# Performance work log

Measured on AMD Instinct MI355X. Metric: run time of the kernel, lower is better.

The kernel has to match this reference:

```python
import jax, jax.numpy as jnp
import numpy as np

EXP, MAN = 8, 23  # exponent/mantissa bits of the simulated float format


def float_quantize(x, exp=EXP, man=MAN):
    """Round-to-nearest-even quantization to a float format with `exp` exponent
    bits and `man` mantissa bits (faithful to mptorch float_quantize 'nearest').
    With exp=8, man=23 this is an exact identity on fp32 inputs."""
    emax = 2 ** (exp - 1) - 1          # max unbiased exponent
    emin = 1 - emax                     # min normal exponent (clamping here yields subnormal grid)
    ax = jnp.abs(x)
    e = jnp.clip(jnp.floor(jnp.log2(jnp.where(ax > 0, ax, 1.0))), emin, emax)
    # scale mantissa into [1,2), round to `man` fractional bits (ties-to-even via jnp.round)
    m = jnp.round(x * jnp.exp2(-e) * (2.0 ** man)) * (2.0 ** -man)
    q = m * jnp.exp2(e)
    maxval = (2.0 - 2.0 ** -man) * (2.0 ** emax)
    q = jnp.clip(q, -maxval, maxval)
    return jnp.where(ax == 0, x, q).astype(x.dtype)


def setup_inputs() -> dict:
    key = jax.random.key(0)
    k1, k2, k3 = jax.random.split(key, 3)
    M, IN, OUT = 8192, 1024, 4096
    x = jax.random.normal(k1, (M, IN), dtype=jnp.float32)
    # kaiming-uniform-ish scale for weight, 1/sqrt(fan_in) for bias
    bound_w = float(np.sqrt(1.0 / IN))
    weight = jax.random.uniform(k2, (OUT, IN), dtype=jnp.float32, minval=-bound_w, maxval=bound_w)
    bias = jax.random.uniform(k3, (OUT,), dtype=jnp.float32, minval=-bound_w, maxval=bound_w)
    return {"x": x, "weight": weight, "bias": bias}


def reference(x, weight, bias):
    # QLinearFunction.forward: quantize weight, quant_gemm, add quantized bias, quantize output.
    # quant_gemm with (man=23, exp=8) simulates fp32 multiply-accumulate, i.e. a plain
    # fp32 GEMM; we express it as matmul followed by output quantization.
    qweight = float_quantize(weight)                 # [OUT, IN]
    out = jnp.matmul(x, qweight.T)                   # [M, OUT], fp32 accumulate
    out = out + float_quantize(bias)[None, :]
    return float_quantize(out)
```

## Files before the change

kernel.cpp:

```cpp
#include <hip/hip_runtime.h>
#include <stdint.h>

#define MM 8192
#define KK 1024
#define NN 4096
#define NT 32
#define TE 8192
#define PL 16384

typedef float f32x4 __attribute__((ext_vector_type(4)));
typedef __bf16 bf16x8 __attribute__((ext_vector_type(8)));
typedef unsigned short u16x8 __attribute__((ext_vector_type(8)));

static __device__ __forceinline__ unsigned short f2bf(float f) {
    unsigned int u = __builtin_bit_cast(unsigned int, f);
    u += 0x7fffu + ((u >> 16) & 1u);
    return (unsigned short)(u >> 16);
}
static __device__ __forceinline__ float bf2f(unsigned short s) {
    unsigned int u = ((unsigned int)s) << 16;
    return __builtin_bit_cast(float, u);
}

__global__ __launch_bounds__(256) void split_pack(const float* __restrict__ in,
        unsigned short* __restrict__ hi, unsigned short* __restrict__ lo, int total) {
    int i = blockIdx.x * 256 + threadIdx.x;
    if (i >= total) return;
    int row = i >> 7;
    int og  = i & 127;
    int kt  = og >> 2, oct = og & 3;
    int bt  = row >> 8, r = row & 255;
    const float4* s = (const float4*)(in + (size_t)row * KK + kt * 32 + oct * 8);
    float4 a = s[0], b = s[1];
    float v[8] = {a.x, a.y, a.z, a.w, b.x, b.y, b.z, b.w};
    u16x8 h, l;
#pragma unroll
    for (int j = 0; j < 8; ++j) {
        unsigned short hb = f2bf(v[j]);
        h[j] = hb;
        l[j] = f2bf(v[j] - bf2f(hb));
    }
    int slot = r * 4 + (oct ^ ((r >> 1) & 3));
    size_t off = (size_t)(bt * NT + kt) * TE + (size_t)slot * 8;
    *(u16x8*)(hi + off) = h;
    *(u16x8*)(lo + off) = l;
}

static __device__ __forceinline__ bf16x8 ldsr(unsigned addr) {
    bf16x8 r;
    asm volatile("ds_read_b128 %0, %1" : "=v"(r) : "v"(addr));
    return r;
}
static __device__ __forceinline__ void gl16(const unsigned short* g, unsigned short* l) {
    __builtin_amdgcn_global_load_lds(
        (__attribute__((address_space(1))) void*)(void*)g,
        (__attribute__((address_space(3))) void*)(void*)l, 16, 0, 0);
}
static __device__ __forceinline__ void mf(f32x4& d, bf16x8 a, bf16x8 b) {
    d = __builtin_amdgcn_mfma_f32_16x16x32_bf16(a, b, d, 0, 0, 0);
}

#define PHASE_PRE() \
    __builtin_amdgcn_s_barrier(); \
    asm volatile("s_waitcnt lgkmcnt(0)" ::: "memory"); \
    __builtin_amdgcn_sched_barrier(0); \
    __builtin_amdgcn_s_setprio(1);
#define PHASE_POST() \
    __builtin_amdgcn_s_setprio(0); \
    __builtin_amdgcn_s_barrier();
#define CLUSTER(M0, M1) \
    _Pragma("unroll") \
    for (int ni = 0; ni < 4; ++ni) { \
        mf(acc[M0][ni], a0, bh[ni]); mf(acc[M0][ni], l0, bh[ni]); mf(acc[M0][ni], a0, blo[ni]); \
        mf(acc[M1][ni], a1, bh[ni]); mf(acc[M1][ni], l1, bh[ni]); mf(acc[M1][ni], a1, blo[ni]); \
    }

__global__ __launch_bounds__(512, 2) void qlinear_mfma(
        const unsigned short* __restrict__ Ah, const unsigned short* __restrict__ Al,
        const unsigned short* __restrict__ Bh, const unsigned short* __restrict__ Bl,
        const float* __restrict__ bias, float* __restrict__ out) {
    __shared__ __attribute__((aligned(16))) unsigned short S[2][4][TE];

    int bid = blockIdx.x;
    int wg = (bid & 7) * 64 + (bid >> 3);
    int bm = wg & 31, bn = wg >> 5;

    const int tix = threadIdx.x;
    const int lane = tix & 63, wid = tix >> 6;
    const int wr = (wid >> 2) * 128, wc = (wid & 3) * 64;
    const int lr = lane & 15, lg = lane >> 4;
    const int xorv = (lr >> 1) & 3;

    const unsigned lb = (unsigned)(uintptr_t)(__attribute__((address_space(3))) void*)&S[0][0][0];
    const unsigned pA = lb + (unsigned)(((wr + lr) * 32 + (lg ^ xorv) * 8) * 2);
    const unsigned pB = lb + (unsigned)(((wc + lr) * 32 + (lg ^ xorv) * 8) * 2);

    const int soff = wid * 1024 + lane * 8;
    const unsigned short* sAh = Ah + (size_t)bm * NT * TE + soff;
    const unsigned short* sAl = Al + (size_t)bm * NT * TE + soff;
    const unsigned short* sBh = Bh + (size_t)bn * NT * TE + soff;
    const unsigned short* sBl = Bl + (size_t)bn * NT * TE + soff;

    f32x4 acc[8][4];
#pragma unroll
    for (int mi = 0; mi < 8; ++mi)
#pragma unroll
        for (int ni = 0; ni < 4; ++ni) acc[mi][ni] = (f32x4){0.f, 0.f, 0.f, 0.f};

    gl16(sAh,       &S[0][0][wid * 1024]);
    gl16(sAh + 512, &S[0][0][wid * 1024 + 512]);
    gl16(sAl,       &S[0][1][wid * 1024]);
    gl16(sAl + 512, &S[0][1][wid * 1024 + 512]);
    gl16(sBh,       &S[0][2][wid * 1024]);
    gl16(sBh + 512, &S[0][2][wid * 1024 + 512]);
    gl16(sBl,       &S[0][3][wid * 1024]);
    gl16(sBl + 512, &S[0][3][wid * 1024 + 512]);
    asm volatile("s_waitcnt vmcnt(0)" ::: "memory");
    __builtin_amdgcn_s_barrier();

    for (int t = 0; t < NT; ++t) {
        const unsigned bo = (unsigned)(t & 1) * (4 * PL);
        const int nb = (t & 1) ^ 1;
        const size_t st = (size_t)(t + 1) * TE;
        const bool pf = (t + 1 < NT);

        bf16x8 bh[4], blo[4], a0, a1, l0, l1;

#pragma unroll
        for (int ni = 0; ni < 4; ++ni) {
            bh[ni]  = ldsr(pB + bo + 2 * PL + ni * 1024);
            blo[ni] = ldsr(pB + bo + 3 * PL + ni * 1024);
        }
        a0 = ldsr(pA + bo);        l0 = ldsr(pA + bo + PL);
        a1 = ldsr(pA + bo + 1024); l1 = ldsr(pA + bo + PL + 1024);
        if (pf) {
            gl16(sAh + st,       &S[nb][0][wid * 1024]);
            gl16(sAh + st + 512, &S[nb][0][wid * 1024 + 512]);
            gl16(sAl + st,       &S[nb][1][wid * 1024]);
            gl16(sAl + st + 512, &S[nb][1][wid * 1024 + 512]);
        }
        PHASE_PRE();
        CLUSTER(0, 1);
        PHASE_POST();

        a0 = ldsr(pA + bo + 2 * 1024); l0 = ldsr(pA + bo + PL + 2 * 1024);
        a1 = ldsr(pA + bo + 3 * 1024); l1 = ldsr(pA + bo + PL + 3 * 1024);
        if (pf) {
            gl16(sBh + st,       &S[nb][2][wid * 1024]);
            gl16(sBh + st + 512, &S[nb][2][wid * 1024 + 512]);
            gl16(sBl + st,       &S[nb][3][wid * 1024]);
            gl16(sBl + st + 512, &S[nb][3][wid * 1024 + 512]);
        }
        PHASE_PRE();
        CLUSTER(2, 3);
        PHASE_POST();

        a0 = ldsr(pA + bo + 4 * 1024); l0 = ldsr(pA + bo + PL + 4 * 1024);
        a1 = ldsr(pA + bo + 5 * 1024); l1 = ldsr(pA + bo + PL + 5 * 1024);
        PHASE_PRE();
        CLUSTER(4, 5);
        PHASE_POST();

        a0 = ldsr(pA + bo + 6 * 1024); l0 = ldsr(pA + bo + PL + 6 * 1024);
        a1 = ldsr(pA + bo + 7 * 1024); l1 = ldsr(pA + bo + PL + 7 * 1024);
        PHASE_PRE();
        CLUSTER(6, 7);
        __builtin_amdgcn_s_setprio(0);
        asm volatile("s_waitcnt vmcnt(0)" ::: "memory");
        __builtin_amdgcn_s_barrier();
    }

    const int row0 = bm * 256 + wr + lg * 4;
    const int col0 = bn * 256 + wc + lr;
    float bv[4];
#pragma unroll
    for (int ni = 0; ni < 4; ++ni) bv[ni] = bias[col0 + ni * 16];
#pragma unroll
    for (int mi = 0; mi < 8; ++mi)
#pragma unroll
        for (int ni = 0; ni < 4; ++ni) {
            float* o = out + (size_t)(row0 + mi * 16) * NN + col0 + ni * 16;
#pragma unroll
            for (int r = 0; r < 4; ++r)
                o[(size_t)r * NN] = acc[mi][ni][r] + bv[ni];
        }
}

__global__ __launch_bounds__(256) void qlinear_naive(const float* __restrict__ x,
                                                     const float* __restrict__ w,
                                                     const float* __restrict__ bias,
                                                     float* __restrict__ out) {
    int n = blockIdx.x * 64 + (threadIdx.x & 63);
    int m = blockIdx.y * 4 + (threadIdx.x >> 6);
    const float4* xr = (const float4*)(x + (size_t)m * KK);
    const float4* wr = (const float4*)(w + (size_t)n * KK);
    float s = 0.f;
    for (int k = 0; k < KK / 4; ++k) {
        float4 a = xr[k], b = wr[k];
        s += a.x * b.x + a.y * b.y + a.z * b.z + a.w * b.w;
    }
    out[(size_t)m * NN + n] = s + bias[n];
}

extern "C" void kernel_launch(void* const* d_in, const int* in_sizes, int n_in,
                              void* d_out, int out_size, void* d_ws, size_t ws_size,
                              hipStream_t stream) {
    (void)in_sizes; (void)n_in; (void)out_size;
    const float* x = (const float*)d_in[0];
    const float* w = (const float*)d_in[1];
    const float* bias = (const float*)d_in[2];
    float* out = (float*)d_out;

    const size_t xcnt = (size_t)MM * KK;
    const size_t wcnt = (size_t)NN * KK;
    const size_t need = (xcnt + wcnt) * 2 * sizeof(unsigned short);

    if (ws_size >= need) {
        unsigned short* xh = (unsigned short*)d_ws;
        unsigned short* xl = xh + xcnt;
        unsigned short* wh = xl + xcnt;
        unsigned short* wl = wh + wcnt;
        split_pack<<<(int)(MM * 128 / 256), 256, 0, stream>>>(x, xh, xl, MM * 128);
        split_pack<<<(int)(NN * 128 / 256), 256, 0, stream>>>(w, wh, wl, NN * 128);
        qlinear_mfma<<<512, 512, 0, stream>>>(xh, xl, wh, wl, bias, out);
    } else {
        dim3 grid(NN / 64, MM / 4);
        qlinear_naive<<<grid, 256, 0, stream>>>(x, w, bias, out);
    }
}
```

Baseline: 335.3 us.

## Switch GEMM to 256x128 tiles with triple-buffered LDS pipeline

Output tiles go from 256x256 to 256x128, so the grid doubles to 1024 blocks and each wave keeps 8x2 accumulators. A three-stage LDS ring issues global loads two K-steps ahead, synchronised with vmcnt waits, replacing double buffering and the per-phase barriers. The split/pack kernel now writes output contiguously and gathers its inputs with swizzled source addresses, so B is packed per 128-row tile. The intent is to hide load latency and cut barrier overhead. In exchange, B reuse per block drops, more of A must be streamed, and occupancy falls to one block per CU.

```diff
diff --git a/kernel.cpp b/kernel.cpp
--- a/kernel.cpp
+++ b/kernel.cpp
@@ -5,8 +5,9 @@
 #define KK 1024
 #define NN 4096
 #define NT 32
-#define TE 8192
-#define PL 16384
+#define TEA 8192
+#define TEB 4096
+#define BUFE 24576
 
 typedef float f32x4 __attribute__((ext_vector_type(4)));
 typedef __bf16 bf16x8 __attribute__((ext_vector_type(8)));
@@ -23,27 +24,28 @@
 }
 
 __global__ __launch_bounds__(256) void split_pack(const float* __restrict__ in,
-        unsigned short* __restrict__ hi, unsigned short* __restrict__ lo, int total) {
-    int i = blockIdx.x * 256 + threadIdx.x;
-    if (i >= total) return;
-    int row = i >> 7;
-    int og  = i & 127;
-    int kt  = og >> 2, oct = og & 3;
-    int bt  = row >> 8, r = row & 255;
-    const float4* s = (const float4*)(in + (size_t)row * KK + kt * 32 + oct * 8);
-    float4 a = s[0], b = s[1];
+        unsigned short* __restrict__ hi, unsigned short* __restrict__ lo,
+        int R, int spl, int total) {
+    int j = blockIdx.x * 256 + threadIdx.x;
+    if (j >= total) return;
+    int p = j >> spl;
+    int s = j & ((R * 4) - 1);
+    int r = s >> 2;
+    int oct = (s & 3) ^ ((r >> 1) & 3);
+    int bt = p >> 5, kt = p & 31;
+    size_t src = (size_t)(bt * R + r) * KK + kt * 32 + oct * 8;
+    const float4* sp = (const float4*)(in + src);
+    float4 a = sp[0], b = sp[1];
     float v[8] = {a.x, a.y, a.z, a.w, b.x, b.y, b.z, b.w};
     u16x8 h, l;
 #pragma unroll
-    for (int j = 0; j < 8; ++j) {
-        unsigned short hb = f2bf(v[j]);
-        h[j] = hb;
-        l[j] = f2bf(v[j] - bf2f(hb));
-    }
-    int slot = r * 4 + (oct ^ ((r >> 1) & 3));
-    size_t off = (size_t)(bt * NT + kt) * TE + (size_t)slot * 8;
-    *(u16x8*)(hi + off) = h;
-    *(u16x8*)(lo + off) = l;
+    for (int q = 0; q < 8; ++q) {
+        unsigned short hb = f2bf(v[q]);
+        h[q] = hb;
+        l[q] = f2bf(v[q] - bf2f(hb));
+    }
+    *(u16x8*)(hi + (size_t)j * 8) = h;
+    *(u16x8*)(lo + (size_t)j * 8) = l;
 }
 
 static __device__ __forceinline__ bf16x8 ldsr(unsigned addr) {
@@ -60,125 +62,113 @@
     d = __builtin_amdgcn_mfma_f32_16x16x32_bf16(a, b, d, 0, 0, 0);
 }
 
-#define PHASE_PRE() \
-    __builtin_amdgcn_s_barrier(); \
-    asm volatile("s_waitcnt lgkmcnt(0)" ::: "memory"); \
-    __builtin_amdgcn_sched_barrier(0); \
-    __builtin_amdgcn_s_setprio(1);
-#define PHASE_POST() \
-    __builtin_amdgcn_s_setprio(0); \
-    __builtin_amdgcn_s_barrier();
-#define CLUSTER(M0, M1) \
-    _Pragma("unroll") \
-    for (int ni = 0; ni < 4; ++ni) { \
-        mf(acc[M0][ni], a0, bh[ni]); mf(acc[M0][ni], l0, bh[ni]); mf(acc[M0][ni], a0, blo[ni]); \
-        mf(acc[M1][ni], a1, bh[ni]); mf(acc[M1][ni], l1, bh[ni]); mf(acc[M1][ni], a1, blo[ni]); \
-    }
-
-__global__ __launch_bounds__(512, 2) void qlinear_mfma(
+__global__ __launch_bounds__(512, 1) void qlinear_mfma(
         const unsigned short* __restrict__ Ah, const unsigned short* __restrict__ Al,
         const unsigned short* __restrict__ Bh, const unsigned short* __restrict__ Bl,
         const float* __restrict__ bias, float* __restrict__ out) {
-    __shared__ __attribute__((aligned(16))) unsigned short S[2][4][TE];
+    __shared__ __attribute__((aligned(16))) unsigned short S[3 * BUFE];
 
     int bid = blockIdx.x;
-    int wg = (bid & 7) * 64 + (bid >> 3);
-    int bm = wg & 31, bn = wg >> 5;
+    int wg = (bid & 7) * 128 + (bid >> 3);
+    int bm = wg >> 5, bn = wg & 31;
 
     const int tix = threadIdx.x;
     const int lane = tix & 63, wid = tix >> 6;
-    const int wr = (wid >> 2) * 128, wc = (wid & 3) * 64;
+    const int wr = (wid >> 2) * 128;
+    const int wc = (wid & 3) * 32;
     const int lr = lane & 15, lg = lane >> 4;
     const int xorv = (lr >> 1) & 3;
 
-    const unsigned lb = (unsigned)(uintptr_t)(__attribute__((address_space(3))) void*)&S[0][0][0];
-    const unsigned pA = lb + (unsigned)(((wr + lr) * 32 + (lg ^ xorv) * 8) * 2);
-    const unsigned pB = lb + (unsigned)(((wc + lr) * 32 + (lg ^ xorv) * 8) * 2);
-
-    const int soff = wid * 1024 + lane * 8;
-    const unsigned short* sAh = Ah + (size_t)bm * NT * TE + soff;
-    const unsigned short* sAl = Al + (size_t)bm * NT * TE + soff;
-    const unsigned short* sBh = Bh + (size_t)bn * NT * TE + soff;
-    const unsigned short* sBl = Bl + (size_t)bn * NT * TE + soff;
-
-    f32x4 acc[8][4];
+    const unsigned lb = (unsigned)(uintptr_t)(__attribute__((address_space(3))) void*)&S[0];
+    const unsigned pA = (unsigned)(((wr + lr) * 32 + (lg ^ xorv) * 8) * 2);
+    const unsigned pB = (unsigned)(((wc + lr) * 32 + (lg ^ xorv) * 8) * 2);
+
+    const unsigned short* pAh = Ah + (size_t)bm * NT * TEA + wid * 1024 + lane * 8;
+    const unsigned short* pAl = Al + (size_t)bm * NT * TEA + wid * 1024 + lane * 8;
+    const unsigned short* pBh = Bh + (size_t)bn * NT * TEB + wid * 512 + lane * 8;
+    const unsigned short* pBl = Bl + (size_t)bn * NT * TEB + wid * 512 + lane * 8;
+
+#define STAGE(T, SOF) do {                                                   \
+        unsigned short* db = &S[(SOF)];                                      \
+        size_t ta = (size_t)(T) * TEA, tb = (size_t)(T) * TEB;               \
+        gl16(pAh + ta,       db + wid * 1024);                               \
+        gl16(pAh + ta + 512, db + wid * 1024 + 512);                         \
+        gl16(pAl + ta,       db + 8192 + wid * 1024);                        \
+        gl16(pAl + ta + 512, db + 8192 + wid * 1024 + 512);                  \
+        gl16(pBh + tb,       db + 16384 + wid * 512);                        \
+        gl16(pBl + tb,       db + 20480 + wid * 512);                        \
+    } while (0)
+
+    f32x4 acc[8][2];
+#pragma unroll
+    for (int mi = 0; mi < 8; ++mi) {
+        acc[mi][0] = (f32x4){0.f, 0.f, 0.f, 0.f};
+        acc[mi][1] = (f32x4){0.f, 0.f, 0.f, 0.f};
+    }
+
+    STAGE(0, 0);
+    STAGE(1, BUFE);
+
+    unsigned roff = 0;
+    unsigned soff = 2 * BUFE;
+
+    for (int t = 0; t < NT; ++t) {
+        if (t == NT - 1) asm volatile("s_waitcnt vmcnt(0)" ::: "memory");
+        else             asm volatile("s_waitcnt vmcnt(6)" ::: "memory");
+        __builtin_amdgcn_s_barrier();
+
+        if (t < NT - 2) STAGE(t + 2, soff);
+
+        const unsigned ab = lb + roff * 2 + pA;
+        const unsigned bb = lb + roff * 2 + 32768 + pB;
+
+        bf16x8 ah[8], al[8], bh2[2], bl2[2];
+        bh2[0] = ldsr(bb);          bh2[1] = ldsr(bb + 1024);
+        bl2[0] = ldsr(bb + 8192);   bl2[1] = ldsr(bb + 8192 + 1024);
+#pragma unroll
+        for (int mi = 0; mi < 4; ++mi) {
+            ah[mi] = ldsr(ab + mi * 1024);
+            al[mi] = ldsr(ab + 16384 + mi * 1024);
+        }
+#pragma unroll
+        for (int mi = 4; mi < 8; ++mi) {
+            ah[mi] = ldsr(ab + mi * 1024);
+            al[mi] = ldsr(ab + 16384 + mi * 1024);
+        }
+
+        asm volatile("s_waitcnt lgkmcnt(8)" ::: "memory");
+        __builtin_amdgcn_sched_barrier(0);
+        __builtin_amdgcn_s_setprio(1);
+#pragma unroll
+        for (int mi = 0; mi < 4; ++mi) { mf(acc[mi][0], ah[mi], bh2[0]); mf(acc[mi][1], ah[mi], bh2[1]); }
+#pragma unroll
+        for (int mi = 0; mi < 4; ++mi) { mf(acc[mi][0], al[mi], bh2[0]); mf(acc[mi][1], al[mi], bh2[1]); }
+#pragma unroll
+        for (int mi = 0; mi < 4; ++mi) { mf(acc[mi][0], ah[mi], bl2[0]); mf(acc[mi][1], ah[mi], bl2[1]); }
+
+        asm volatile("s_waitcnt lgkmcnt(0)" ::: "memory");
+        __builtin_amdgcn_sched_barrier(0);
+#pragma unroll
+        for (int mi = 4; mi < 8; ++mi) { mf(acc[mi][0], ah[mi], bh2[0]); mf(acc[mi][1], ah[mi], bh2[1]); }
+#pragma unroll
+        for (int mi = 4; mi < 8; ++mi) { mf(acc[mi][0], al[mi], bh2[0]); mf(acc[mi][1], al[mi], bh2[1]); }
+#pragma unroll
+        for (int mi = 4; mi < 8; ++mi) { mf(acc[mi][0], ah[mi], bl2[0]); mf(acc[mi][1], ah[mi], bl2[1]); }
+        __builtin_amdgcn_s_setprio(0);
+        __builtin_amdgcn_sched_barrier(0);
+
+        roff = (roff == 2 * BUFE) ? 0u : roff + BUFE;
+        soff = (soff == 2 * BUFE) ? 0u : soff + BUFE;
+    }
+#undef STAGE
+
+    const int row0 = bm * 256 + wr + lg * 4;
+    const int col0 = bn * 128 + wc + lr;
+    float bv[2] = {bias[col0], bias[col0 + 16]};
 #pragma unroll
     for (int mi = 0; mi < 8; ++mi)
 #pragma unroll
-        for (int ni = 0; ni < 4; ++ni) acc[mi][ni] = (f32x4){0.f, 0.f, 0.f, 0.f};
-
-    gl16(sAh,       &S[0][0][wid * 1024]);
-    gl16(sAh + 512, &S[0][0][wid * 1024 + 512]);
-    gl16(sAl,       &S[0][1][wid * 1024]);
-    gl16(sAl + 512, &S[0][1][wid * 1024 + 512]);
-    gl16(sBh,       &S[0][2][wid * 1024]);
-    gl16(sBh + 512, &S[0][2][wid * 1024 + 512]);
-    gl16(sBl,       &S[0][3][wid * 1024]);
-    gl16(sBl + 512, &S[0][3][wid * 1024 + 512]);
-    asm volatile("s_waitcnt vmcnt(0)" ::: "memory");
-    __builtin_amdgcn_s_barrier();
-
-    for (int t = 0; t < NT; ++t) {
-        const unsigned bo = (unsigned)(t & 1) * (4 * PL);
-        const int nb = (t & 1) ^ 1;
-        const size_t st = (size_t)(t + 1) * TE;
-        const bool pf = (t + 1 < NT);
-
-        bf16x8 bh[4], blo[4], a0, a1, l0, l1;
-
-#pragma unroll
-        for (int ni = 0; ni < 4; ++ni) {
-            bh[ni]  = ldsr(pB + bo + 2 * PL + ni * 1024);
-            blo[ni] = ldsr(pB + bo + 3 * PL + ni * 1024);
-        }
-        a0 = ldsr(pA + bo);        l0 = ldsr(pA + bo + PL);
-        a1 = ldsr(pA + bo + 1024); l1 = ldsr(pA + bo + PL + 1024);
-        if (pf) {
-            gl16(sAh + st,       &S[nb][0][wid * 1024]);
-            gl16(sAh + st + 512, &S[nb][0][wid * 1024 + 512]);
-            gl16(sAl + st,       &S[nb][1][wid * 1024]);
-            gl16(sAl + st + 512, &S[nb][1][wid * 1024 + 512]);
-        }
-        PHASE_PRE();
-        CLUSTER(0, 1);
-        PHASE_POST();
-
-        a0 = ldsr(pA + bo + 2 * 1024); l0 = ldsr(pA + bo + PL + 2 * 1024);
-        a1 = ldsr(pA + bo + 3 * 1024); l1 = ldsr(pA + bo + PL + 3 * 1024);
-        if (pf) {
-            gl16(sBh + st,       &S[nb][2][wid * 1024]);
-            gl16(sBh + st + 512, &S[nb][2][wid * 1024 + 512]);
-            gl16(sBl + st,       &S[nb][3][wid * 1024]);
-            gl16(sBl + st + 512, &S[nb][3][wid * 1024 + 512]);
-        }
-        PHASE_PRE();
-        CLUSTER(2, 3);
-        PHASE_POST();
-
-        a0 = ldsr(pA + bo + 4 * 1024); l0 = ldsr(pA + bo + PL + 4 * 1024);
-        a1 = ldsr(pA + bo + 5 * 1024); l1 = ldsr(pA + bo + PL + 5 * 1024);
-        PHASE_PRE();
-        CLUSTER(4, 5);
-        PHASE_POST();
-
-        a0 = ldsr(pA + bo + 6 * 1024); l0 = ldsr(pA + bo + PL + 6 * 1024);
-        a1 = ldsr(pA + bo + 7 * 1024); l1 = ldsr(pA + bo + PL + 7 * 1024);
-        PHASE_PRE();
-        CLUSTER(6, 7);
-        __builtin_amdgcn_s_setprio(0);
-        asm volatile("s_waitcnt vmcnt(0)" ::: "memory");
-        __builtin_amdgcn_s_barrier();
-    }
-
-    const int row0 = bm * 256 + wr + lg * 4;
-    const int col0 = bn * 256 + wc + lr;
-    float bv[4];
-#pragma unroll
-    for (int ni = 0; ni < 4; ++ni) bv[ni] = bias[col0 + ni * 16];
-#pragma unroll
-    for (int mi = 0; mi < 8; ++mi)
-#pragma unroll
-        for (int ni = 0; ni < 4; ++ni) {
+        for (int ni = 0; ni < 2; ++ni) {
             float* o = out + (size_t)(row0 + mi * 16) * NN + col0 + ni * 16;
 #pragma unroll
             for (int r = 0; r < 4; ++r)
@@ -220,9 +210,9 @@
         unsigned short* xl = xh + xcnt;
         unsigned short* wh = xl + xcnt;
         unsigned short* wl = wh + wcnt;
-        split_pack<<<(int)(MM * 128 / 256), 256, 0, stream>>>(x, xh, xl, MM * 128);
-        split_pack<<<(int)(NN * 128 / 256), 256, 0, stream>>>(w, wh, wl, NN * 128);
-        qlinear_mfma<<<512, 512, 0, stream>>>(xh, xl, wh, wl, bias, out);
+        split_pack<<<(int)(xcnt / 8 / 256), 256, 0, stream>>>(x, xh, xl, 256, 10, (int)(xcnt / 8));
+        split_pack<<<(int)(wcnt / 8 / 256), 256, 0, stream>>>(w, wh, wl, 128, 9, (int)(wcnt / 8));
+        qlinear_mfma<<<1024, 512, 0, stream>>>(xh, xl, wh, wl, bias, out);
     } else {
         dim3 grid(NN / 64, MM / 4);
         qlinear_naive<<<grid, 256, 0, stream>>>(x, w, bias, out);
```

Measured after the change: 327.3 us. -2.4%, faster.
